# Performance work log

Hardware: AMD Instinct MI355X
Metric: run time of the kernel (lower is better)

## Reference

```python
import jax, jax.numpy as jnp
import numpy as np

B, S, HID = 2, 2048, 1024
H, D = 16, 64
NUM_BUCKETS, MAX_DIST = 32, 128
NEG_INF = -1e9


def _rel_buckets(rel_pos, num_buckets, max_distance):
    # decoder (unidirectional): only non-positive relative positions valid
    rp = -jnp.minimum(rel_pos, 0)  # [q,k] >= 0
    max_exact = num_buckets // 2
    is_small = rp < max_exact
    safe = jnp.maximum(rp, 1).astype(jnp.float32)
    large = max_exact + (
        jnp.log(safe / max_exact) / np.log(max_distance / max_exact) * (num_buckets - max_exact)
    ).astype(jnp.int32)
    large = jnp.minimum(large, num_buckets - 1)
    return jnp.where(is_small, rp, large)


def _rotate_half(t):
    t1, t2 = jnp.split(t, 2, axis=-1)
    return jnp.concatenate([-t2, t1], axis=-1)


def setup_inputs() -> dict:
    key = jax.random.key(0)
    ks = jax.random.split(key, 6)
    sc = 0.02
    x = jax.random.normal(ks[0], (B, S, HID), jnp.float32)
    Wq = jax.random.normal(ks[1], (HID, H * D), jnp.float32) * sc
    Wk = jax.random.normal(ks[2], (HID, H * D), jnp.float32) * sc
    Wv = jax.random.normal(ks[3], (HID, H * D), jnp.float32) * sc
    Wo = jax.random.normal(ks[4], (H * D, HID), jnp.float32) * sc
    rel_bias = jax.random.normal(ks[5], (NUM_BUCKETS, H), jnp.float32) * sc
    # rotary tables: emb = cat(freqs, freqs), non-interleave layout
    inv_freq = 1.0 / (10000.0 ** (np.arange(0, D, 2, dtype=np.float32) / D))
    freqs = np.arange(S, dtype=np.float32)[:, None] * inv_freq[None, :]  # [S, D/2]
    emb = np.concatenate([freqs, freqs], axis=-1)  # [S, D]
    cos = jnp.asarray(np.cos(emb), jnp.float32)
    sin = jnp.asarray(np.sin(emb), jnp.float32)
    return {"x": x, "Wq": Wq, "Wk": Wk, "Wv": Wv, "Wo": Wo,
            "rel_bias": rel_bias, "cos": cos, "sin": sin}


def reference(x, Wq, Wk, Wv, Wo, rel_bias, cos, sin):
    # QKV projections (weights stored [in, out])
    q = (x @ Wq).reshape(B, S, H, D)
    k = (x @ Wk).reshape(B, S, H, D)
    v = (x @ Wv).reshape(B, S, H, D)
    # RoPE (non-interleave): q*cos + rotate_half(q)*sin, cos/sin broadcast over B,H
    c = cos[None, :, None, :]
    s = sin[None, :, None, :]
    q = q * c + _rotate_half(q) * s
    k = k * c + _rotate_half(k) * s
    # scores [B,H,S,S]
    scores = jnp.einsum("bqhd,bkhd->bhqk", q, k) / np.sqrt(D).astype(np.float32)
    # learned relative-position bucket bias (T5-style, decoder/unidirectional)
    ctx_pos = jnp.arange(S)[:, None]
    mem_pos = jnp.arange(S)[None, :]
    buckets = _rel_buckets(mem_pos - ctx_pos, NUM_BUCKETS, MAX_DIST)  # [S,S]
    bias = rel_bias[buckets]  # [S,S,H]
    scores = scores + jnp.transpose(bias, (2, 0, 1))[None]
    # causal mask (decoder self-attention)
    causal = mem_pos <= ctx_pos  # [S,S]
    scores = jnp.where(causal[None, None], scores, NEG_INF)
    attn = jax.nn.softmax(scores, axis=-1)
    ctx = jnp.einsum("bhqk,bkhd->bqhd", attn, v).reshape(B, S, H * D)
    return ctx @ Wo
```

## Files before the change

### kernel.cpp

```cpp
#include <hip/hip_runtime.h>
#include <hip/hip_bf16.h>
#include <math.h>

#define B_   2
#define S_   2048
#define HID_ 1024
#define H_   16
#define D_   64
#define HD_  (H_ * D_)

typedef __attribute__((ext_vector_type(8))) short bf16x8;
typedef __attribute__((ext_vector_type(4))) short bf16x4;
typedef __attribute__((ext_vector_type(4))) float f32x4;
typedef __attribute__((ext_vector_type(4))) unsigned uint4v;
typedef unsigned short u16;

#define LOG2E 1.44269504088896f

static __device__ __forceinline__ u16 f2bf(float f) {
    unsigned u = __builtin_bit_cast(unsigned, f);
    u += 0x7fffu + ((u >> 16) & 1u);
    return (u16)(u >> 16);
}
static __device__ __forceinline__ unsigned cvtpk(float lo, float hi) {
    unsigned r;
    asm("v_cvt_pk_bf16_f32 %0, %1, %2" : "=v"(r) : "v"(lo), "v"(hi));
    return r;
}
static __device__ __forceinline__ int swzK(int row, int colbytes) {
    return row * 128 + (colbytes ^ ((row & 7) << 4));
}
static __device__ __forceinline__ int swzV(int row, int colbytes) {
    return row * 128 + (colbytes ^ ((row & 7) << 4) ^ (((row >> 3) & 1) << 3));
}
static __device__ __forceinline__ void gll16(const void* g, void* l) {
    __builtin_amdgcn_global_load_lds(
        (const __attribute__((address_space(1))) unsigned int*)g,
        (__attribute__((address_space(3))) unsigned int*)l, 16, 0, 0);
}

__global__ __launch_bounds__(256) void prep(const float* __restrict__ x,
                                            u16* __restrict__ xb,
                                            const float* __restrict__ W0,
                                            const float* __restrict__ W1,
                                            const float* __restrict__ W2,
                                            const float* __restrict__ W3,
                                            u16* __restrict__ o0,
                                            u16* __restrict__ o1,
                                            u16* __restrict__ o2,
                                            u16* __restrict__ o3) {
    __shared__ float tS[32][33];
    const int bid = blockIdx.x;
    if (bid < 4096) {
        int i = bid * 256 + threadIdx.x;
        float4 f = ((const float4*)x)[i];
        ushort4 u;
        u.x = f2bf(f.x); u.y = f2bf(f.y); u.z = f2bf(f.z); u.w = f2bf(f.w);
        ((ushort4*)xb)[i] = u;
    } else {
        const int id  = bid - 4096;
        const int z   = id >> 10;
        const int rem = id & 1023;
        const float* in = z == 0 ? W0 : z == 1 ? W1 : z == 2 ? W2 : W3;
        u16* out       = z == 0 ? o0 : z == 1 ? o1 : z == 2 ? o2 : o3;
        const int bx = (rem & 31) * 32, by = (rem >> 5) * 32;
        const int xx = threadIdx.x & 31, yy = threadIdx.x >> 5;
        #pragma unroll
        for (int j = 0; j < 4; j++)
            tS[yy + j * 8][xx] = in[(long)(by + yy + j * 8) * HID_ + bx + xx];
        __syncthreads();
        #pragma unroll
        for (int j = 0; j < 4; j++)
            out[(long)(bx + yy + j * 8) * HID_ + by + xx] = f2bf(tS[xx][yy + j * 8]);
    }
}

__global__ __launch_bounds__(256, 3) void gemm_qkv(const u16* __restrict__ A,
                                                   const u16* __restrict__ Bt,
                                                   u16* __restrict__ outb,
                                                   const float* __restrict__ cosb,
                                                   const float* __restrict__ sinb,
                                                   int K) {
    __shared__ u16 As[128 * 64];
    __shared__ u16 Bs[128 * 64];
    const int t = threadIdx.x;
    const int lane = t & 63;
    const int w = t >> 6;
    const int qlane = lane & 15, grp = lane >> 4;
    const int m0 = blockIdx.y * 128, n0 = blockIdx.x * 128;
    const int wr = w >> 1, wc = w & 1;

    f32x4 acc[4][4];
    #pragma unroll
    for (int i = 0; i < 4; i++)
        #pragma unroll
        for (int j = 0; j < 4; j++) acc[i][j] = (f32x4){0.f, 0.f, 0.f, 0.f};

    const int srow = lane >> 3;
    const int scol = ((lane & 7) ^ srow) * 8;
    const int swa  = (qlane & 7) << 4;
    const int nkt = K >> 6;
    for (int kt = 0; kt < nkt; kt++) {
        const int k0 = kt << 6;
        #pragma unroll
        for (int c = 0; c < 4; c++) {
            const int chunk = w * 4 + c;
            const int row = chunk * 8 + srow;
            gll16(A  + (long)(m0 + row) * K + k0 + scol, As + chunk * 512);
            gll16(Bt + (long)(n0 + row) * K + k0 + scol, Bs + chunk * 512);
        }
        __syncthreads();
        #pragma unroll
        for (int ks = 0; ks < 2; ks++) {
            bf16x8 af[4], bfr[4];
            #pragma unroll
            for (int i = 0; i < 4; i++) {
                af[i]  = *(const bf16x8*)((const unsigned char*)As
                         + (wr * 64 + i * 16 + qlane) * 128 + ((ks * 64 + grp * 16) ^ swa));
                bfr[i] = *(const bf16x8*)((const unsigned char*)Bs
                         + (wc * 64 + i * 16 + qlane) * 128 + ((ks * 64 + grp * 16) ^ swa));
            }
            #pragma unroll
            for (int mf = 0; mf < 4; mf++)
                #pragma unroll
                for (int nf = 0; nf < 4; nf++)
                    acc[mf][nf] = __builtin_amdgcn_mfma_f32_16x16x32_bf16(bfr[nf], af[mf], acc[mf][nf], 0, 0, 0);
        }
        __syncthreads();
    }

    const int gnb = n0 + wc * 64;
    const bool isqk = gnb < 2048;
    const bool isq  = gnb < 1024;
    const float QS = 0.125f * LOG2E;
    #pragma unroll
    for (int mf = 0; mf < 4; mf++) {
        const int m = m0 + wr * 64 + mf * 16 + qlane;
        if (isqk) {
            const int s = m & (S_ - 1);
            const float* cr = cosb + s * 64;
            const float* sr = sinb + s * 64;
            #pragma unroll
            for (int nf2 = 0; nf2 < 2; nf2++) {
                #pragma unroll
                for (int r = 0; r < 4; r++) {
                    const int d = nf2 * 16 + grp * 4 + r;
                    float lo = acc[mf][nf2][r], hi = acc[mf][nf2 + 2][r];
                    float nlo = lo * cr[d]      - hi * sr[d];
                    float nhi = hi * cr[d + 32] + lo * sr[d + 32];
                    if (isq) { nlo *= QS; nhi *= QS; }
                    acc[mf][nf2][r]     = nlo;
                    acc[mf][nf2 + 2][r] = nhi;
                }
            }
        }
        #pragma unroll
        for (int nf = 0; nf < 4; nf++) {
            const int gn = gnb + nf * 16 + grp * 4;
            ushort4 o4;
            o4.x = f2bf(acc[mf][nf][0]); o4.y = f2bf(acc[mf][nf][1]);
            o4.z = f2bf(acc[mf][nf][2]); o4.w = f2bf(acc[mf][nf][3]);
            *(ushort4*)&outb[((long)(gn >> 10)) * ((long)4096 * 1024) + (long)m * 1024 + (gn & 1023)] = o4;
        }
    }
}

__global__ __launch_bounds__(256, 3) void gemm_n64(const u16* __restrict__ A,
                                                   const u16* __restrict__ Bt,
                                                   float* __restrict__ outf,
                                                   int K) {
    __shared__ u16 As[128 * 64];
    __shared__ u16 Bs[64 * 64];
    const int t = threadIdx.x;
    const int lane = t & 63;
    const int w = t >> 6;
    const int qlane = lane & 15, grp = lane >> 4;
    const int m0 = blockIdx.y * 128, n0 = blockIdx.x * 64;

    f32x4 acc[2][4];
    #pragma unroll
    for (int i = 0; i < 2; i++)
        #pragma unroll
        for (int j = 0; j < 4; j++) acc[i][j] = (f32x4){0.f, 0.f, 0.f, 0.f};

    const int srow = lane >> 3;
    const int scol = ((lane & 7) ^ srow) * 8;
    const int swa  = (qlane & 7) << 4;
    const int nkt = K >> 6;
    for (int kt = 0; kt < nkt; kt++) {
        const int k0 = kt << 6;
        #pragma unroll
        for (int c = 0; c < 4; c++) {
            const int chunk = w * 4 + c;
            gll16(A + (long)(m0 + chunk * 8 + srow) * K + k0 + scol, As + chunk * 512);
        }
        #pragma unroll
        for (int c = 0; c < 2; c++) {
            const int chunk = w * 2 + c;
            gll16(Bt + (long)(n0 + chunk * 8 + srow) * K + k0 + scol, Bs + chunk * 512);
        }
        __syncthreads();
        #pragma unroll
        for (int ks = 0; ks < 2; ks++) {
            bf16x8 af[2], bfr[4];
            #pragma unroll
            for (int i = 0; i < 2; i++)
                af[i] = *(const bf16x8*)((const unsigned char*)As
                        + (w * 32 + i * 16 + qlane) * 128 + ((ks * 64 + grp * 16) ^ swa));
            #pragma unroll
            for (int i = 0; i < 4; i++)
                bfr[i] = *(const bf16x8*)((const unsigned char*)Bs
                         + (i * 16 + qlane) * 128 + ((ks * 64 + grp * 16) ^ swa));
            #pragma unroll
            for (int mf = 0; mf < 2; mf++)
                #pragma unroll
                for (int nf = 0; nf < 4; nf++)
                    acc[mf][nf] = __builtin_amdgcn_mfma_f32_16x16x32_bf16(bfr[nf], af[mf], acc[mf][nf], 0, 0, 0);
        }
        __syncthreads();
    }

    #pragma unroll
    for (int mf = 0; mf < 2; mf++) {
        const int m = m0 + w * 32 + mf * 16 + qlane;
        #pragma unroll
        for (int nf = 0; nf < 4; nf++) {
            float4 o4;
            o4.x = acc[mf][nf][0]; o4.y = acc[mf][nf][1];
            o4.z = acc[mf][nf][2]; o4.w = acc[mf][nf][3];
            *(float4*)&outf[(long)m * 1024 + n0 + nf * 16 + grp * 4] = o4;
        }
    }
}

__global__ __launch_bounds__(512, 4) void attn_mfma(const u16* __restrict__ q,
                                                    const u16* __restrict__ k,
                                                    const u16* __restrict__ v,
                                                    const float* __restrict__ rel_bias,
                                                    u16* __restrict__ ctx) {
    __shared__ __align__(16) unsigned char kS[2][8192];
    __shared__ __align__(16) unsigned char vS[2][8192];
    __shared__ float bb[2][192];

    const int t    = threadIdx.x;
    const int lane = t & 63;
    const int w    = t >> 6;
    const int n    = blockIdx.x;
    const int xcd  = n & 7;
    const int hbhi = (n >> 7) & 3;
    int qtb        = (n >> 3) & 15;
    if (hbhi & 2) qtb = 15 - qtb;
    const int hb   = xcd + (hbhi << 3);
    const int h    = hb & 15, b = hb >> 4;
    const int q0   = qtb * 128;
    const int wq   = w * 16;
    const int qwq  = q0 + wq;
    const int qlane = lane & 15;
    const int grp   = lane >> 4;

    const long bhbase = ((long)b * S_ * H_ + h) * D_;
    const float bfar  = rel_bias[31 * H_ + h] * LOG2E;

    const int kr  = t >> 3,        kc  = (t & 7) * 8;
    const int vrb = (t >> 5) * 4,  vcp = (t & 31) * 2;

    bf16x8 qf0, qf1;
    {
        const u16* qrow = q + bhbase + (long)(qwq + qlane) * HD_;
        qf0 = *(const bf16x8*)(qrow + grp * 8);
        qf1 = *(const bf16x8*)(qrow + 32 + grp * 8);
    }

    f32x4 oacc[4];
    #pragma unroll
    for (int db = 0; db < 4; db++) oacc[db] = (f32x4){0.f, 0.f, 0.f, 0.f};
    float m_run = -1.0e30f, l_run = 0.f;

    bf16x8 kreg;
    unsigned vreg[4];
    float breg = 0.f;

    auto prefetch = [&](int k0, bool needb) {
        kreg = *(const bf16x8*)(k + bhbase + (long)(k0 + kr) * HD_ + kc);
        const u16* vp = v + bhbase + (long)(k0 + vrb) * HD_ + vcp;
        #pragma unroll
        for (int i = 0; i < 4; i++)
            vreg[i] = *(const unsigned*)(vp + (long)i * HD_);
        if (needb && t < 192) {
            int rp = (q0 - 63) + t - k0;
            float bv = 0.f;
            if (rp >= 0) {
                int bucket;
                if (rp < 16) bucket = rp;
                else {
                    int lg = (int)(logf((float)rp * 0.0625f) * 7.69437361f);
                    bucket = 16 + lg;
                    if (bucket > 31) bucket = 31;
                }
                bv = rel_bias[bucket * H_ + h] * LOG2E;
            }
            breg = bv;
        }
    };
    auto writetile = [&](int buf, bool needb) {
        *(bf16x8*)(kS[buf] + swzK(kr, kc * 2)) = kreg;
        ushort2 a0 = __builtin_bit_cast(ushort2, vreg[0]);
        ushort2 a1 = __builtin_bit_cast(ushort2, vreg[1]);
        ushort2 a2 = __builtin_bit_cast(ushort2, vreg[2]);
        ushort2 a3 = __builtin_bit_cast(ushort2, vreg[3]);
        ushort4 d0; d0.x = a0.x; d0.y = a1.x; d0.z = a2.x; d0.w = a3.x;
        ushort4 d1; d1.x = a0.y; d1.y = a1.y; d1.z = a2.y; d1.w = a3.y;
        *(ushort4*)(vS[buf] + swzV(vcp,     vrb * 2)) = d0;
        *(ushort4*)(vS[buf] + swzV(vcp + 1, vrb * 2)) = d1;
        if (needb && t < 192) bb[buf][t] = breg;
    };

    const int NT = 2 * qtb + 2;
    const bool needb0 = (q0 < 176);
    prefetch(0, needb0);
    writetile(0, needb0);
    __syncthreads();

    int cur = 0;
    for (int kt = 0; kt < NT; kt++) {
        const int k0 = kt * 64;
        const bool has_next = (kt + 1) < NT;
        const bool needb_n  = (q0 - (k0 + 64)) < 176;
        if (has_next) prefetch(k0 + 64, needb_n);

        const bool skip = k0 > qwq + 15;
        if (!skip) {
            const bool use_bias = (qwq - k0) < 176;
            const bool is_diag  = (k0 + 63) > qwq;

            __builtin_amdgcn_s_setprio(1);
            f32x4 sacc[4];
            #pragma unroll
            for (int kb = 0; kb < 4; kb++) {
                sacc[kb] = (f32x4){0.f, 0.f, 0.f, 0.f};
                bf16x8 kf0 = *(const bf16x8*)(kS[cur] + swzK(kb * 16 + qlane, grp * 16));
                bf16x8 kf1 = *(const bf16x8*)(kS[cur] + swzK(kb * 16 + qlane, 64 + grp * 16));
                sacc[kb] = __builtin_amdgcn_mfma_f32_16x16x32_bf16(kf0, qf0, sacc[kb], 0, 0, 0);
                sacc[kb] = __builtin_amdgcn_mfma_f32_16x16x32_bf16(kf1, qf1, sacc[kb], 0, 0, 0);
            }
            __builtin_amdgcn_s_setprio(0);

            float pv_[4][4];
            float tmax = -1.0e30f;
            #pragma unroll
            for (int kb = 0; kb < 4; kb++) {
                #pragma unroll
                for (int r = 0; r < 4; r++) {
                    float s = sacc[kb][r];
                    if (use_bias) {
                        const int k_l = kb * 16 + grp * 4 + r;
                        s += bb[cur][wq + qlane - k_l + 63];
                        if (is_diag)
                            s = ((k0 + k_l) <= (qwq + qlane)) ? s : -1.0e9f;
                    }
                    pv_[kb][r] = s;
                }
                tmax = fmaxf(tmax,
                       fmaxf(fmaxf(pv_[kb][0], pv_[kb][1]), fmaxf(pv_[kb][2], pv_[kb][3])));
            }
            tmax = fmaxf(tmax, __shfl_xor(tmax, 16));
            tmax = fmaxf(tmax, __shfl_xor(tmax, 32));

            const float bofs = use_bias ? 0.f : bfar;
            const float teff = tmax + bofs;
            float msub;
            if (__all(teff <= m_run + 11.5f)) {
                msub = m_run - bofs;
            } else {
                float mnew  = fmaxf(m_run, teff);
                float scale = __builtin_amdgcn_exp2f(m_run - mnew);
                l_run *= scale;
                #pragma unroll
                for (int db = 0; db < 4; db++)
                    #pragma unroll
                    for (int r = 0; r < 4; r++) oacc[db][r] *= scale;
                m_run = mnew;
                msub = mnew - bofs;
            }

            float tsum = 0.f;
            #pragma unroll
            for (int kb = 0; kb < 4; kb++)
                #pragma unroll
                for (int r = 0; r < 4; r++) {
                    float p = __builtin_amdgcn_exp2f(pv_[kb][r] - msub);
                    pv_[kb][r] = p;
                    tsum += p;
                }
            tsum += __shfl_xor(tsum, 16);
            tsum += __shfl_xor(tsum, 32);
            l_run += tsum;

            bf16x8 pf[2];
            #pragma unroll
            for (int ks = 0; ks < 2; ks++) {
                unsigned u0 = cvtpk(pv_[2 * ks][0], pv_[2 * ks][1]);
                unsigned u1 = cvtpk(pv_[2 * ks][2], pv_[2 * ks][3]);
                unsigned u2 = cvtpk(pv_[2 * ks + 1][0], pv_[2 * ks + 1][1]);
                unsigned u3 = cvtpk(pv_[2 * ks + 1][2], pv_[2 * ks + 1][3]);
                pf[ks] = __builtin_bit_cast(bf16x8, (uint4v){u0, u1, u2, u3});
            }

            __builtin_amdgcn_s_setprio(1);
            #pragma unroll
            for (int db = 0; db < 4; db++) {
                #pragma unroll
                for (int ks = 0; ks < 2; ks++) {
                    bf16x4 lo = *(const bf16x4*)(vS[cur] + swzV(db * 16 + qlane, ks * 64 + grp * 8));
                    bf16x4 hi = *(const bf16x4*)(vS[cur] + swzV(db * 16 + qlane, ks * 64 + 32 + grp * 8));
                    bf16x8 vf = __builtin_shufflevector(lo, hi, 0, 1, 2, 3, 4, 5, 6, 7);
                    oacc[db] = __builtin_amdgcn_mfma_f32_16x16x32_bf16(vf, pf[ks], oacc[db], 0, 0, 0);
                }
            }
            __builtin_amdgcn_s_setprio(0);
        }

        if (has_next) writetile(cur ^ 1, needb_n);
        __syncthreads();
        cur ^= 1;
    }

    const float inv = 1.0f / l_run;
    u16* dst = ctx + (long)(b * S_ + qwq + qlane) * HID_ + h * D_;
    #pragma unroll
    for (int db = 0; db < 4; db++) {
        ushort4 o4;
        o4.x = f2bf(oacc[db][0] * inv);
        o4.y = f2bf(oacc[db][1] * inv);
        o4.z = f2bf(oacc[db][2] * inv);
        o4.w = f2bf(oacc[db][3] * inv);
        *(ushort4*)(dst + db * 16 + grp * 4) = o4;
    }
}

extern "C" void kernel_launch(void* const* d_in, const int* in_sizes, int n_in,
                              void* d_out, int out_size, void* d_ws, size_t ws_size,
                              hipStream_t stream) {
    const float* x    = (const float*)d_in[0];
    const float* Wq   = (const float*)d_in[1];
    const float* Wk   = (const float*)d_in[2];
    const float* Wv   = (const float*)d_in[3];
    const float* Wo   = (const float*)d_in[4];
    const float* rb   = (const float*)d_in[5];
    const float* cosb = (const float*)d_in[6];
    const float* sinb = (const float*)d_in[7];
    float* out = (float*)d_out;

    char* wsb = (char*)d_ws;
    u16* xb    = (u16*)(wsb);
    u16* wqkvT = (u16*)(wsb + (8L  << 20));
    u16* woT   = (u16*)(wsb + (14L << 20));
    u16* qb    = (u16*)(wsb + (16L << 20));
    u16* kb    = (u16*)(wsb + (24L << 20));
    u16* vb    = (u16*)(wsb + (32L << 20));
    u16* ctxb  = (u16*)(wsb + (40L << 20));

    hipLaunchKernelGGL(prep, dim3(4096 + 4096), dim3(256), 0, stream,
                       x, xb, Wq, Wk, Wv, Wo,
                       wqkvT, wqkvT + (1L << 20), wqkvT + (2L << 20), woT);
    hipLaunchKernelGGL(gemm_qkv, dim3(24, 32), dim3(256), 0, stream,
                       xb, wqkvT, qb, cosb, sinb, HID_);
    hipLaunchKernelGGL(attn_mfma, dim3(512), dim3(512), 0, stream,
                       qb, kb, vb, rb, ctxb);
    hipLaunchKernelGGL(gemm_n64, dim3(16, 32), dim3(256), 0, stream,
                       ctxb, woT, out, HID_);
}
```

Measured before the change: 117.4 us.

## Halve attention query tile to 64 rows with 256-thread blocks and rebalanced schedule

```diff
diff --git a/kernel.cpp b/kernel.cpp
--- a/kernel.cpp
+++ b/kernel.cpp
@@ -233,26 +233,32 @@
     }
 }
 
-__global__ __launch_bounds__(512, 4) void attn_mfma(const u16* __restrict__ q,
+__global__ __launch_bounds__(256, 4) void attn_mfma(const u16* __restrict__ q,
                                                     const u16* __restrict__ k,
                                                     const u16* __restrict__ v,
                                                     const float* __restrict__ rel_bias,
                                                     u16* __restrict__ ctx) {
     __shared__ __align__(16) unsigned char kS[2][8192];
     __shared__ __align__(16) unsigned char vS[2][8192];
-    __shared__ float bb[2][192];
+    __shared__ float bb[2][128];
 
     const int t    = threadIdx.x;
     const int lane = t & 63;
     const int w    = t >> 6;
     const int n    = blockIdx.x;
     const int xcd  = n & 7;
-    const int hbhi = (n >> 7) & 3;
-    int qtb        = (n >> 3) & 15;
-    if (hbhi & 2) qtb = 15 - qtb;
+    const int j    = (n >> 3) & 31;
+    const int hbhi = (n >> 8) & 3;
+    int qt;
+    switch (hbhi) {
+        case 0: qt = j; break;
+        case 1: qt = 31 - j; break;
+        case 2: qt = (j + 8) & 31; break;
+        default: qt = 31 - ((j + 8) & 31); break;
+    }
     const int hb   = xcd + (hbhi << 3);
     const int h    = hb & 15, b = hb >> 4;
-    const int q0   = qtb * 128;
+    const int q0   = qt * 64;
     const int wq   = w * 16;
     const int qwq  = q0 + wq;
     const int qlane = lane & 15;
@@ -260,9 +266,6 @@
 
     const long bhbase = ((long)b * S_ * H_ + h) * D_;
     const float bfar  = rel_bias[31 * H_ + h] * LOG2E;
-
-    const int kr  = t >> 3,        kc  = (t & 7) * 8;
-    const int vrb = (t >> 5) * 4,  vcp = (t & 31) * 2;
 
     bf16x8 qf0, qf1;
     {
@@ -276,17 +279,23 @@
     for (int db = 0; db < 4; db++) oacc[db] = (f32x4){0.f, 0.f, 0.f, 0.f};
     float m_run = -1.0e30f, l_run = 0.f;
 
-    bf16x8 kreg;
-    unsigned vreg[4];
+    bf16x8 kreg[2];
+    unsigned vreg[8];
     float breg = 0.f;
 
     auto prefetch = [&](int k0, bool needb) {
-        kreg = *(const bf16x8*)(k + bhbase + (long)(k0 + kr) * HD_ + kc);
-        const u16* vp = v + bhbase + (long)(k0 + vrb) * HD_ + vcp;
-        #pragma unroll
-        for (int i = 0; i < 4; i++)
-            vreg[i] = *(const unsigned*)(vp + (long)i * HD_);
-        if (needb && t < 192) {
+        #pragma unroll
+        for (int i = 0; i < 2; i++) {
+            const int u  = t + i * 256;
+            const int kr = u >> 3, kc = (u & 7) * 8;
+            kreg[i] = *(const bf16x8*)(k + bhbase + (long)(k0 + kr) * HD_ + kc);
+            const int vrb = (u >> 5) * 4, vcp = (u & 31) * 2;
+            const u16* vp = v + bhbase + (long)(k0 + vrb) * HD_ + vcp;
+            #pragma unroll
+            for (int i2 = 0; i2 < 4; i2++)
+                vreg[i * 4 + i2] = *(const unsigned*)(vp + (long)i2 * HD_);
+        }
+        if (needb && t < 128) {
             int rp = (q0 - 63) + t - k0;
             float bv = 0.f;
             if (rp >= 0) {
@@ -303,19 +312,25 @@
         }
     };
     auto writetile = [&](int buf, bool needb) {
-        *(bf16x8*)(kS[buf] + swzK(kr, kc * 2)) = kreg;
-        ushort2 a0 = __builtin_bit_cast(ushort2, vreg[0]);
-        ushort2 a1 = __builtin_bit_cast(ushort2, vreg[1]);
-        ushort2 a2 = __builtin_bit_cast(ushort2, vreg[2]);
-        ushort2 a3 = __builtin_bit_cast(ushort2, vreg[3]);
-        ushort4 d0; d0.x = a0.x; d0.y = a1.x; d0.z = a2.x; d0.w = a3.x;
-        ushort4 d1; d1.x = a0.y; d1.y = a1.y; d1.z = a2.y; d1.w = a3.y;
-        *(ushort4*)(vS[buf] + swzV(vcp,     vrb * 2)) = d0;
-        *(ushort4*)(vS[buf] + swzV(vcp + 1, vrb * 2)) = d1;
-        if (needb && t < 192) bb[buf][t] = breg;
+        #pragma unroll
+        for (int i = 0; i < 2; i++) {
+            const int u  = t + i * 256;
+            const int kr = u >> 3, kc = (u & 7) * 8;
+            *(bf16x8*)(kS[buf] + swzK(kr, kc * 2)) = kreg[i];
+            const int vrb = (u >> 5) * 4, vcp = (u & 31) * 2;
+            ushort2 a0 = __builtin_bit_cast(ushort2, vreg[i * 4 + 0]);
+            ushort2 a1 = __builtin_bit_cast(ushort2, vreg[i * 4 + 1]);
+            ushort2 a2 = __builtin_bit_cast(ushort2, vreg[i * 4 + 2]);
+            ushort2 a3 = __builtin_bit_cast(ushort2, vreg[i * 4 + 3]);
+            ushort4 d0; d0.x = a0.x; d0.y = a1.x; d0.z = a2.x; d0.w = a3.x;
+            ushort4 d1; d1.x = a0.y; d1.y = a1.y; d1.z = a2.y; d1.w = a3.y;
+            *(ushort4*)(vS[buf] + swzV(vcp,     vrb * 2)) = d0;
+            *(ushort4*)(vS[buf] + swzV(vcp + 1, vrb * 2)) = d1;
+        }
+        if (needb && t < 128) bb[buf][t] = breg;
     };
 
-    const int NT = 2 * qtb + 2;
+    const int NT = qt + 1;
     const bool needb0 = (q0 < 176);
     prefetch(0, needb0);
     writetile(0, needb0);
@@ -328,97 +343,94 @@
         const bool needb_n  = (q0 - (k0 + 64)) < 176;
         if (has_next) prefetch(k0 + 64, needb_n);
 
-        const bool skip = k0 > qwq + 15;
-        if (!skip) {
-            const bool use_bias = (qwq - k0) < 176;
-            const bool is_diag  = (k0 + 63) > qwq;
-
-            __builtin_amdgcn_s_setprio(1);
-            f32x4 sacc[4];
-            #pragma unroll
-            for (int kb = 0; kb < 4; kb++) {
-                sacc[kb] = (f32x4){0.f, 0.f, 0.f, 0.f};
-                bf16x8 kf0 = *(const bf16x8*)(kS[cur] + swzK(kb * 16 + qlane, grp * 16));
-                bf16x8 kf1 = *(const bf16x8*)(kS[cur] + swzK(kb * 16 + qlane, 64 + grp * 16));
-                sacc[kb] = __builtin_amdgcn_mfma_f32_16x16x32_bf16(kf0, qf0, sacc[kb], 0, 0, 0);
-                sacc[kb] = __builtin_amdgcn_mfma_f32_16x16x32_bf16(kf1, qf1, sacc[kb], 0, 0, 0);
-            }
-            __builtin_amdgcn_s_setprio(0);
-
-            float pv_[4][4];
-            float tmax = -1.0e30f;
-            #pragma unroll
-            for (int kb = 0; kb < 4; kb++) {
+        const bool use_bias = (qwq - k0) < 176;
+        const bool is_diag  = (k0 + 63) > qwq;
+
+        __builtin_amdgcn_s_setprio(1);
+        f32x4 sacc[4];
+        #pragma unroll
+        for (int kb = 0; kb < 4; kb++) {
+            sacc[kb] = (f32x4){0.f, 0.f, 0.f, 0.f};
+            bf16x8 kf0 = *(const bf16x8*)(kS[cur] + swzK(kb * 16 + qlane, grp * 16));
+            bf16x8 kf1 = *(const bf16x8*)(kS[cur] + swzK(kb * 16 + qlane, 64 + grp * 16));
+            sacc[kb] = __builtin_amdgcn_mfma_f32_16x16x32_bf16(kf0, qf0, sacc[kb], 0, 0, 0);
+            sacc[kb] = __builtin_amdgcn_mfma_f32_16x16x32_bf16(kf1, qf1, sacc[kb], 0, 0, 0);
+        }
+        __builtin_amdgcn_s_setprio(0);
+
+        float pv_[4][4];
+        float tmax = -1.0e30f;
+        #pragma unroll
+        for (int kb = 0; kb < 4; kb++) {
+            #pragma unroll
+            for (int r = 0; r < 4; r++) {
+                float s = sacc[kb][r];
+                if (use_bias) {
+                    const int k_l = kb * 16 + grp * 4 + r;
+                    s += bb[cur][wq + qlane - k_l + 63];
+                    if (is_diag)
+                        s = ((k0 + k_l) <= (qwq + qlane)) ? s : -1.0e9f;
+                }
+                pv_[kb][r] = s;
+            }
+            tmax = fmaxf(tmax,
+                   fmaxf(fmaxf(pv_[kb][0], pv_[kb][1]), fmaxf(pv_[kb][2], pv_[kb][3])));
+        }
+        tmax = fmaxf(tmax, __shfl_xor(tmax, 16));
+        tmax = fmaxf(tmax, __shfl_xor(tmax, 32));
+
+        const float bofs = use_bias ? 0.f : bfar;
+        const float teff = tmax + bofs;
+        float msub;
+        if (__all(teff <= m_run + 11.5f)) {
+            msub = m_run - bofs;
+        } else {
+            float mnew  = fmaxf(m_run, teff);
+            float scale = __builtin_amdgcn_exp2f(m_run - mnew);
+            l_run *= scale;
+            #pragma unroll
+            for (int db = 0; db < 4; db++)
                 #pragma unroll
-                for (int r = 0; r < 4; r++) {
-                    float s = sacc[kb][r];
-                    if (use_bias) {
-                        const int k_l = kb * 16 + grp * 4 + r;
-                        s += bb[cur][wq + qlane - k_l + 63];
-                        if (is_diag)
-                            s = ((k0 + k_l) <= (qwq + qlane)) ? s : -1.0e9f;
-                    }
-                    pv_[kb][r] = s;
-                }
-                tmax = fmaxf(tmax,
-                       fmaxf(fmaxf(pv_[kb][0], pv_[kb][1]), fmaxf(pv_[kb][2], pv_[kb][3])));
-            }
-            tmax = fmaxf(tmax, __shfl_xor(tmax, 16));
-            tmax = fmaxf(tmax, __shfl_xor(tmax, 32));
-
-            const float bofs = use_bias ? 0.f : bfar;
-            const float teff = tmax + bofs;
-            float msub;
-            if (__all(teff <= m_run + 11.5f)) {
-                msub = m_run - bofs;
-            } else {
-                float mnew  = fmaxf(m_run, teff);
-                float scale = __builtin_amdgcn_exp2f(m_run - mnew);
-                l_run *= scale;
-                #pragma unroll
-                for (int db = 0; db < 4; db++)
-                    #pragma unroll
-                    for (int r = 0; r < 4; r++) oacc[db][r] *= scale;
-                m_run = mnew;
-                msub = mnew - bofs;
-            }
-
-            float tsum = 0.f;
-            #pragma unroll
-            for (int kb = 0; kb < 4; kb++)
-                #pragma unroll
-                for (int r = 0; r < 4; r++) {
-                    float p = __builtin_amdgcn_exp2f(pv_[kb][r] - msub);
-                    pv_[kb][r] = p;
-                    tsum += p;
-                }
-            tsum += __shfl_xor(tsum, 16);
-            tsum += __shfl_xor(tsum, 32);
-            l_run += tsum;
-
-            bf16x8 pf[2];
+                for (int r = 0; r < 4; r++) oacc[db][r] *= scale;
+            m_run = mnew;
+            msub = mnew - bofs;
+        }
+
+        float tsum = 0.f;
+        #pragma unroll
+        for (int kb = 0; kb < 4; kb++)
+            #pragma unroll
+            for (int r = 0; r < 4; r++) {
+                float p = __builtin_amdgcn_exp2f(pv_[kb][r] - msub);
+                pv_[kb][r] = p;
+                tsum += p;
+            }
+        tsum += __shfl_xor(tsum, 16);
+        tsum += __shfl_xor(tsum, 32);
+        l_run += tsum;
+
+        bf16x8 pf[2];
+        #pragma unroll
+        for (int ks = 0; ks < 2; ks++) {
+            unsigned u0 = cvtpk(pv_[2 * ks][0], pv_[2 * ks][1]);
+            unsigned u1 = cvtpk(pv_[2 * ks][2], pv_[2 * ks][3]);
+            unsigned u2 = cvtpk(pv_[2 * ks + 1][0], pv_[2 * ks + 1][1]);
+            unsigned u3 = cvtpk(pv_[2 * ks + 1][2], pv_[2 * ks + 1][3]);
+            pf[ks] = __builtin_bit_cast(bf16x8, (uint4v){u0, u1, u2, u3});
+        }
+
+        __builtin_amdgcn_s_setprio(1);
+        #pragma unroll
+        for (int db = 0; db < 4; db++) {
             #pragma unroll
             for (int ks = 0; ks < 2; ks++) {
-                unsigned u0 = cvtpk(pv_[2 * ks][0], pv_[2 * ks][1]);
-                unsigned u1 = cvtpk(pv_[2 * ks][2], pv_[2 * ks][3]);
-                unsigned u2 = cvtpk(pv_[2 * ks + 1][0], pv_[2 * ks + 1][1]);
-                unsigned u3 = cvtpk(pv_[2 * ks + 1][2], pv_[2 * ks + 1][3]);
-                pf[ks] = __builtin_bit_cast(bf16x8, (uint4v){u0, u1, u2, u3});
-            }
-
-            __builtin_amdgcn_s_setprio(1);
-            #pragma unroll
-            for (int db = 0; db < 4; db++) {
-                #pragma unroll
-                for (int ks = 0; ks < 2; ks++) {
-                    bf16x4 lo = *(const bf16x4*)(vS[cur] + swzV(db * 16 + qlane, ks * 64 + grp * 8));
-                    bf16x4 hi = *(const bf16x4*)(vS[cur] + swzV(db * 16 + qlane, ks * 64 + 32 + grp * 8));
-                    bf16x8 vf = __builtin_shufflevector(lo, hi, 0, 1, 2, 3, 4, 5, 6, 7);
-                    oacc[db] = __builtin_amdgcn_mfma_f32_16x16x32_bf16(vf, pf[ks], oacc[db], 0, 0, 0);
-                }
-            }
-            __builtin_amdgcn_s_setprio(0);
-        }
+                bf16x4 lo = *(const bf16x4*)(vS[cur] + swzV(db * 16 + qlane, ks * 64 + grp * 8));
+                bf16x4 hi = *(const bf16x4*)(vS[cur] + swzV(db * 16 + qlane, ks * 64 + 32 + grp * 8));
+                bf16x8 vf = __builtin_shufflevector(lo, hi, 0, 1, 2, 3, 4, 5, 6, 7);
+                oacc[db] = __builtin_amdgcn_mfma_f32_16x16x32_bf16(vf, pf[ks], oacc[db], 0, 0, 0);
+            }
+        }
+        __builtin_amdgcn_s_setprio(0);
 
         if (has_next) writetile(cur ^ 1, needb_n);
         __syncthreads();
@@ -465,7 +477,7 @@
                        wqkvT, wqkvT + (1L << 20), wqkvT + (2L << 20), woT);
     hipLaunchKernelGGL(gemm_qkv, dim3(24, 32), dim3(256), 0, stream,
                        xb, wqkvT, qb, cosb, sinb, HID_);
-    hipLaunchKernelGGL(attn_mfma, dim3(512), dim3(512), 0, stream,
+    hipLaunchKernelGGL(attn_mfma, dim3(1024), dim3(256), 0, stream,
                        qb, kb, vb, rb, ctxb);
     hipLaunchKernelGGL(gemm_n64, dim3(16, 32), dim3(256), 0, stream,
                        ctxb, woT, out, HID_);
```

Result: no change. 118.2 us (+0.7%).

## Stage two 64-key subtiles per barrier in attention loop

Applied to the files above, without the earlier changes.

```diff
diff --git a/kernel.cpp b/kernel.cpp
--- a/kernel.cpp
+++ b/kernel.cpp
@@ -238,9 +238,9 @@
                                                     const u16* __restrict__ v,
                                                     const float* __restrict__ rel_bias,
                                                     u16* __restrict__ ctx) {
-    __shared__ __align__(16) unsigned char kS[2][8192];
-    __shared__ __align__(16) unsigned char vS[2][8192];
-    __shared__ float bb[2][192];
+    __shared__ __align__(16) unsigned char kS[2][2][8192];
+    __shared__ __align__(16) unsigned char vS[2][2][8192];
+    __shared__ float bb[2][256];
 
     const int t    = threadIdx.x;
     const int lane = t & 63;
@@ -276,18 +276,22 @@
     for (int db = 0; db < 4; db++) oacc[db] = (f32x4){0.f, 0.f, 0.f, 0.f};
     float m_run = -1.0e30f, l_run = 0.f;
 
-    bf16x8 kreg;
-    unsigned vreg[4];
+    bf16x8 kregA, kregB;
+    unsigned vreg[8];
     float breg = 0.f;
 
-    auto prefetch = [&](int k0, bool needb) {
-        kreg = *(const bf16x8*)(k + bhbase + (long)(k0 + kr) * HD_ + kc);
-        const u16* vp = v + bhbase + (long)(k0 + vrb) * HD_ + vcp;
-        #pragma unroll
-        for (int i = 0; i < 4; i++)
-            vreg[i] = *(const unsigned*)(vp + (long)i * HD_);
-        if (needb && t < 192) {
-            int rp = (q0 - 63) + t - k0;
+    auto prefetch = [&](int k0p, bool needb) {
+        const u16* kp = k + bhbase + (long)(k0p + kr) * HD_ + kc;
+        kregA = *(const bf16x8*)kp;
+        kregB = *(const bf16x8*)(kp + (long)64 * HD_);
+        const u16* vp = v + bhbase + (long)(k0p + vrb) * HD_ + vcp;
+        #pragma unroll
+        for (int i = 0; i < 4; i++) {
+            vreg[i]     = *(const unsigned*)(vp + (long)i * HD_);
+            vreg[i + 4] = *(const unsigned*)(vp + (long)(i + 64) * HD_);
+        }
+        if (needb && t < 256) {
+            int rp = q0 - k0p - 127 + t;
             float bv = 0.f;
             if (rp >= 0) {
                 int bucket;
@@ -303,43 +307,48 @@
         }
     };
     auto writetile = [&](int buf, bool needb) {
-        *(bf16x8*)(kS[buf] + swzK(kr, kc * 2)) = kreg;
-        ushort2 a0 = __builtin_bit_cast(ushort2, vreg[0]);
-        ushort2 a1 = __builtin_bit_cast(ushort2, vreg[1]);
-        ushort2 a2 = __builtin_bit_cast(ushort2, vreg[2]);
-        ushort2 a3 = __builtin_bit_cast(ushort2, vreg[3]);
-        ushort4 d0; d0.x = a0.x; d0.y = a1.x; d0.z = a2.x; d0.w = a3.x;
-        ushort4 d1; d1.x = a0.y; d1.y = a1.y; d1.z = a2.y; d1.w = a3.y;
-        *(ushort4*)(vS[buf] + swzV(vcp,     vrb * 2)) = d0;
-        *(ushort4*)(vS[buf] + swzV(vcp + 1, vrb * 2)) = d1;
-        if (needb && t < 192) bb[buf][t] = breg;
+        *(bf16x8*)(kS[buf][0] + swzK(kr, kc * 2)) = kregA;
+        *(bf16x8*)(kS[buf][1] + swzK(kr, kc * 2)) = kregB;
+        #pragma unroll
+        for (int s = 0; s < 2; s++) {
+            ushort2 a0 = __builtin_bit_cast(ushort2, vreg[s * 4 + 0]);
+            ushort2 a1 = __builtin_bit_cast(ushort2, vreg[s * 4 + 1]);
+            ushort2 a2 = __builtin_bit_cast(ushort2, vreg[s * 4 + 2]);
+            ushort2 a3 = __builtin_bit_cast(ushort2, vreg[s * 4 + 3]);
+            ushort4 d0; d0.x = a0.x; d0.y = a1.x; d0.z = a2.x; d0.w = a3.x;
+            ushort4 d1; d1.x = a0.y; d1.y = a1.y; d1.z = a2.y; d1.w = a3.y;
+            *(ushort4*)(vS[buf][s] + swzV(vcp,     vrb * 2)) = d0;
+            *(ushort4*)(vS[buf][s] + swzV(vcp + 1, vrb * 2)) = d1;
+        }
+        if (needb && t < 256) bb[buf][t] = breg;
     };
 
-    const int NT = 2 * qtb + 2;
-    const bool needb0 = (q0 < 176);
-    prefetch(0, needb0);
-    writetile(0, needb0);
+    const int NPAIR = qtb + 1;
+    prefetch(0, q0 < 256);
+    writetile(0, q0 < 256);
     __syncthreads();
 
     int cur = 0;
-    for (int kt = 0; kt < NT; kt++) {
-        const int k0 = kt * 64;
-        const bool has_next = (kt + 1) < NT;
-        const bool needb_n  = (q0 - (k0 + 64)) < 176;
-        if (has_next) prefetch(k0 + 64, needb_n);
-
-        const bool skip = k0 > qwq + 15;
-        if (!skip) {
-            const bool use_bias = (qwq - k0) < 176;
-            const bool is_diag  = (k0 + 63) > qwq;
+    for (int pr = 0; pr < NPAIR; pr++) {
+        const int k0p = pr * 128;
+        const bool has_next = (pr + 1) < NPAIR;
+        const bool needb_n  = (q0 - (k0p + 128)) < 256;
+        if (has_next) prefetch(k0p + 128, needb_n);
+
+        #pragma unroll
+        for (int sub = 0; sub < 2; sub++) {
+            const int k0s = k0p + sub * 64;
+            if (k0s > qwq + 15) break;
+            const bool use_bias = (qwq - k0s) < 176;
+            const bool is_diag  = (k0s + 63) > qwq;
 
             __builtin_amdgcn_s_setprio(1);
             f32x4 sacc[4];
             #pragma unroll
             for (int kb = 0; kb < 4; kb++) {
                 sacc[kb] = (f32x4){0.f, 0.f, 0.f, 0.f};
-                bf16x8 kf0 = *(const bf16x8*)(kS[cur] + swzK(kb * 16 + qlane, grp * 16));
-                bf16x8 kf1 = *(const bf16x8*)(kS[cur] + swzK(kb * 16 + qlane, 64 + grp * 16));
+                bf16x8 kf0 = *(const bf16x8*)(kS[cur][sub] + swzK(kb * 16 + qlane, grp * 16));
+                bf16x8 kf1 = *(const bf16x8*)(kS[cur][sub] + swzK(kb * 16 + qlane, 64 + grp * 16));
                 sacc[kb] = __builtin_amdgcn_mfma_f32_16x16x32_bf16(kf0, qf0, sacc[kb], 0, 0, 0);
                 sacc[kb] = __builtin_amdgcn_mfma_f32_16x16x32_bf16(kf1, qf1, sacc[kb], 0, 0, 0);
             }
@@ -354,9 +363,9 @@
                     float s = sacc[kb][r];
                     if (use_bias) {
                         const int k_l = kb * 16 + grp * 4 + r;
-                        s += bb[cur][wq + qlane - k_l + 63];
+                        s += bb[cur][wq + qlane - sub * 64 - k_l + 127];
                         if (is_diag)
-                            s = ((k0 + k_l) <= (qwq + qlane)) ? s : -1.0e9f;
+                            s = ((k0s + k_l) <= (qwq + qlane)) ? s : -1.0e9f;
                     }
                     pv_[kb][r] = s;
                 }
@@ -411,8 +420,8 @@
             for (int db = 0; db < 4; db++) {
                 #pragma unroll
                 for (int ks = 0; ks < 2; ks++) {
-                    bf16x4 lo = *(const bf16x4*)(vS[cur] + swzV(db * 16 + qlane, ks * 64 + grp * 8));
-                    bf16x4 hi = *(const bf16x4*)(vS[cur] + swzV(db * 16 + qlane, ks * 64 + 32 + grp * 8));
+                    bf16x4 lo = *(const bf16x4*)(vS[cur][sub] + swzV(db * 16 + qlane, ks * 64 + grp * 8));
+                    bf16x4 hi = *(const bf16x4*)(vS[cur][sub] + swzV(db * 16 + qlane, ks * 64 + 32 + grp * 8));
                     bf16x8 vf = __builtin_shufflevector(lo, hi, 0, 1, 2, 3, 4, 5, 6, 7);
                     oacc[db] = __builtin_amdgcn_mfma_f32_16x16x32_bf16(vf, pf[ks], oacc[db], 0, 0, 0);
                 }
```

Measured after the change: 120.6 us. +2.7%, slower.
